# Performance work log

Hardware: AMD Instinct MI355X
Metric: run time of the kernel (lower is better)

## Reference

```python
import jax, jax.numpy as jnp
import numpy as np

HEADS = 8
MAX_REL = 256
D_MODEL = 512
QK_DIM = 512
V_DIM = 512
HEAD_QK = QK_DIM // HEADS
HEAD_V = V_DIM // HEADS
NUM_RPR = 2 * MAX_REL + 1


def setup_inputs() -> dict:
    key = jax.random.key(0)
    ks = jax.random.split(key, 9)
    B, S = 2, 2048
    scale = 1.0 / np.sqrt(D_MODEL)
    return {
        "query": jax.random.normal(ks[0], (B, S, D_MODEL), jnp.float32),
        "value": jax.random.normal(ks[1], (B, S, D_MODEL), jnp.float32),
        "Wq": jax.random.normal(ks[2], (D_MODEL, QK_DIM), jnp.float32) * scale,
        "Wk": jax.random.normal(ks[3], (D_MODEL, QK_DIM), jnp.float32) * scale,
        "Wv": jax.random.normal(ks[4], (D_MODEL, V_DIM), jnp.float32) * scale,
        "Wo": jax.random.normal(ks[5], (V_DIM, D_MODEL), jnp.float32) * scale,
        "bo": jnp.zeros((D_MODEL,), jnp.float32),
        "Ek": jax.random.normal(ks[6], (NUM_RPR, HEAD_QK), jnp.float32) * 0.02,
        "Ev": jax.random.normal(ks[7], (NUM_RPR, HEAD_V), jnp.float32) * 0.02,
    }


def _heads(x, h):
    B, S, D = x.shape
    return x.reshape(B, S, h, D // h).transpose(0, 2, 1, 3)  # (B,H,S,hd)


def reference(query, value, Wq, Wk, Wv, Wo, bo, Ek, Ev):
    B, S, _ = query.shape
    # rpr lookup: clip(j - i, -M, M) + M  -> (S, S)
    idx = jnp.arange(S)
    rpr = jnp.clip(idx[None, :] - idx[:, None], -MAX_REL, MAX_REL) + MAX_REL
    ek = Ek[rpr]  # (S, S, head_qk)
    ev = Ev[rpr]  # (S, S, head_v)

    q = _heads(query @ Wq, HEADS)   # (B,H,S,dk)
    k = _heads(value @ Wk, HEADS)   # key := value (per original call())
    v = _heads(value @ Wv, HEADS)   # (B,H,S,dv)

    alpha = jnp.einsum("bhid,bhjd->bhij", q, k)
    alpha = alpha + jnp.einsum("bhid,ijd->bhij", q, ek)
    alpha = alpha / jnp.sqrt(jnp.asarray(HEAD_QK, jnp.float32))
    attn_weights = jax.nn.softmax(alpha, axis=-1)  # (B,H,S,S)

    scores = jnp.einsum("bhij,bhjd->bhid", attn_weights, v)
    scores = scores + jnp.einsum("bhij,ijd->bhid", attn_weights, ev)

    concat = scores.transpose(0, 2, 1, 3).reshape(B, S, V_DIM)
    out = concat @ Wo + bo
    return out, attn_weights
```

## Files before the change

### kernel.cpp

```cpp
#include <hip/hip_runtime.h>

#define SB 2
#define HH 8
#define SS 2048
#define DM 512
#define HD 64
#define SCALE 0.125f

typedef __attribute__((ext_vector_type(8))) short bfrag;
typedef __attribute__((ext_vector_type(4))) float f4;

static __device__ __forceinline__ unsigned short f2bf(float x) {
  unsigned int u = __float_as_uint(x);
  unsigned int r = (u + 0x7FFFu + ((u >> 16) & 1u)) >> 16;
  return (unsigned short)r;
}
static __device__ __forceinline__ float bf2f(unsigned short s) {
  return __uint_as_float(((unsigned int)s) << 16);
}
static __device__ __forceinline__ void splitf(float x, short& hi, short& lo) {
  const unsigned u = __float_as_uint(x);
  hi = (short)(u >> 16);
  lo = (short)f2bf(x - __uint_as_float(u & 0xFFFF0000u));
}

static __device__ __forceinline__ void dma16(const unsigned short* g,
                                             unsigned short* l) {
  __builtin_amdgcn_global_load_lds(
      (const __attribute__((address_space(1))) void*)g,
      (__attribute__((address_space(3))) void*)l, 16, 0, 0);
}
static __device__ __forceinline__ void wait_vm4() {
  asm volatile("s_waitcnt vmcnt(4)" ::: "memory");
  __builtin_amdgcn_sched_barrier(0);
}
static __device__ __forceinline__ void wait_vm0() {
  asm volatile("s_waitcnt vmcnt(0)" ::: "memory");
  __builtin_amdgcn_sched_barrier(0);
}

__global__ __launch_bounds__(256) void gemm_f32(const float* __restrict__ A,
                                                const float* __restrict__ Bm,
                                                const float* __restrict__ bias,
                                                float* __restrict__ C,
                                                int M, int N, int K) {
  __shared__ float As[16][68];
  __shared__ float Bs[16][64];
  const int t = threadIdx.x;
  const int nb = N >> 6;
  const int bm = blockIdx.x / nb, bn = blockIdx.x % nb;
  const int m0 = bm << 6, n0 = bn << 6;
  const int ty = t >> 4, tx = t & 15;
  const int mr = ty << 2, nc = tx << 2;
  const int am = t >> 2, akq = t & 3;
  const int bk = t >> 4, bnq = t & 15;
  float acc[4][4] = {};
  for (int k0 = 0; k0 < K; k0 += 16) {
    const float4 av = *(const float4*)&A[(size_t)(m0 + am) * K + k0 + (akq << 2)];
    const float4 bv = *(const float4*)&Bm[(size_t)(k0 + bk) * N + n0 + (bnq << 2)];
    __syncthreads();
    As[(akq << 2) + 0][am] = av.x;
    As[(akq << 2) + 1][am] = av.y;
    As[(akq << 2) + 2][am] = av.z;
    As[(akq << 2) + 3][am] = av.w;
    *(float4*)&Bs[bk][bnq << 2] = bv;
    __syncthreads();
#pragma unroll
    for (int kk = 0; kk < 16; ++kk) {
      float a[4], b[4];
      *(float4*)a = *(const float4*)&As[kk][mr];
      *(float4*)b = *(const float4*)&Bs[kk][nc];
#pragma unroll
      for (int i = 0; i < 4; ++i)
#pragma unroll
        for (int j = 0; j < 4; ++j) acc[i][j] += a[i] * b[j];
    }
  }
#pragma unroll
  for (int i = 0; i < 4; ++i) {
    float4 v = make_float4(acc[i][0], acc[i][1], acc[i][2], acc[i][3]);
    if (bias) {
      v.x += bias[n0 + nc + 0];
      v.y += bias[n0 + nc + 1];
      v.z += bias[n0 + nc + 2];
      v.w += bias[n0 + nc + 3];
    }
    *(float4*)&C[(size_t)(m0 + mr + i) * N + n0 + nc] = v;
  }
}

__global__ __launch_bounds__(256) void gemm_f32_vt(const float* __restrict__ A,
                                                   const float* __restrict__ Bm,
                                                   unsigned short* __restrict__ VT,
                                                   int M, int N, int K) {
  __shared__ float As[16][68];
  __shared__ float Bs[16][64];
  const int t = threadIdx.x;
  const int nb = N >> 6;
  const int bm = blockIdx.x / nb, bn = blockIdx.x % nb;
  const int m0 = bm << 6, n0 = bn << 6;
  const int ty = t >> 4, tx = t & 15;
  const int mr = ty << 2, nc = tx << 2;
  const int am = t >> 2, akq = t & 3;
  const int bk = t >> 4, bnq = t & 15;
  float acc[4][4] = {};
  for (int k0 = 0; k0 < K; k0 += 16) {
    const float4 av = *(const float4*)&A[(size_t)(m0 + am) * K + k0 + (akq << 2)];
    const float4 bv = *(const float4*)&Bm[(size_t)(k0 + bk) * N + n0 + (bnq << 2)];
    __syncthreads();
    As[(akq << 2) + 0][am] = av.x;
    As[(akq << 2) + 1][am] = av.y;
    As[(akq << 2) + 2][am] = av.z;
    As[(akq << 2) + 3][am] = av.w;
    *(float4*)&Bs[bk][bnq << 2] = bv;
    __syncthreads();
#pragma unroll
    for (int kk = 0; kk < 16; ++kk) {
      float a[4], b[4];
      *(float4*)a = *(const float4*)&As[kk][mr];
      *(float4*)b = *(const float4*)&Bs[kk][nc];
#pragma unroll
      for (int i = 0; i < 4; ++i)
#pragma unroll
        for (int j = 0; j < 4; ++j) acc[i][j] += a[i] * b[j];
    }
  }
#pragma unroll
  for (int i = 0; i < 4; ++i) {
    const int row = m0 + mr + i;
    const int bb = row >> 11, jr = row & 2047;
#pragma unroll
    for (int jx = 0; jx < 4; ++jx) {
      const int col = n0 + nc + jx;
      const int bh = bb * HH + (col >> 6), d = col & 63;
      VT[((size_t)bh * HD + d) * SS + jr] = f2bf(acc[i][jx]);
    }
  }
}

__global__ __launch_bounds__(256) void gemm_f32_khl(const float* __restrict__ A,
                                                    const float* __restrict__ Bm,
                                                    unsigned short* __restrict__ kh,
                                                    unsigned short* __restrict__ kl,
                                                    int M, int N, int K) {
  __shared__ float As[16][68];
  __shared__ float Bs[16][64];
  const int t = threadIdx.x;
  const int nb = N >> 6;
  const int bm = blockIdx.x / nb, bn = blockIdx.x % nb;
  const int m0 = bm << 6, n0 = bn << 6;
  const int ty = t >> 4, tx = t & 15;
  const int mr = ty << 2, nc = tx << 2;
  const int am = t >> 2, akq = t & 3;
  const int bk = t >> 4, bnq = t & 15;
  float acc[4][4] = {};
  for (int k0 = 0; k0 < K; k0 += 16) {
    const float4 av = *(const float4*)&A[(size_t)(m0 + am) * K + k0 + (akq << 2)];
    const float4 bv = *(const float4*)&Bm[(size_t)(k0 + bk) * N + n0 + (bnq << 2)];
    __syncthreads();
    As[(akq << 2) + 0][am] = av.x;
    As[(akq << 2) + 1][am] = av.y;
    As[(akq << 2) + 2][am] = av.z;
    As[(akq << 2) + 3][am] = av.w;
    *(float4*)&Bs[bk][bnq << 2] = bv;
    __syncthreads();
#pragma unroll
    for (int kk = 0; kk < 16; ++kk) {
      float a[4], b[4];
      *(float4*)a = *(const float4*)&As[kk][mr];
      *(float4*)b = *(const float4*)&Bs[kk][nc];
#pragma unroll
      for (int i = 0; i < 4; ++i)
#pragma unroll
        for (int j = 0; j < 4; ++j) acc[i][j] += a[i] * b[j];
    }
  }
#pragma unroll
  for (int i = 0; i < 4; ++i) {
    const int row = m0 + mr + i;
    const int bb = row >> 11, jr = row & 2047;
#pragma unroll
    for (int jx = 0; jx < 4; ++jx) {
      const int col = n0 + nc + jx;
      const int bh = bb * HH + (col >> 6), d = col & 63;
      short hi, lo;
      splitf(acc[i][jx], hi, lo);
      const size_t o = ((size_t)bh * SS + jr) * HD + d;
      kh[o] = (unsigned short)hi;
      kl[o] = (unsigned short)lo;
    }
  }
}

__global__ void prep_evt(const float* __restrict__ Ev, unsigned short* __restrict__ EvT) {
  const int idx = blockIdx.x * 256 + threadIdx.x;
  if (idx >= 64 * 544) return;
  const int d = idx / 544, r = idx % 544;
  EvT[idx] = (r < 513) ? f2bf(Ev[(size_t)r * HD + d]) : (unsigned short)0;
}

#define QK6(K0, K1, L0, L1, ACC)                                            \
  ACC = __builtin_amdgcn_mfma_f32_16x16x32_bf16(qh0, K0, ACC, 0, 0, 0);     \
  ACC = __builtin_amdgcn_mfma_f32_16x16x32_bf16(qh1, K1, ACC, 0, 0, 0);     \
  ACC = __builtin_amdgcn_mfma_f32_16x16x32_bf16(ql0, K0, ACC, 0, 0, 0);     \
  ACC = __builtin_amdgcn_mfma_f32_16x16x32_bf16(ql1, K1, ACC, 0, 0, 0);     \
  ACC = __builtin_amdgcn_mfma_f32_16x16x32_bf16(qh0, L0, ACC, 0, 0, 0);     \
  ACC = __builtin_amdgcn_mfma_f32_16x16x32_bf16(qh1, L1, ACC, 0, 0, 0);

__global__ __launch_bounds__(256, 2) void fused_attn10(
    const float* __restrict__ Qp,
    const unsigned short* __restrict__ khg,
    const unsigned short* __restrict__ klg,
    const unsigned short* __restrict__ VTg,
    const float* __restrict__ Ek,
    const unsigned short* __restrict__ EvT,
    float* __restrict__ attn,
    float* __restrict__ concat) {
  __shared__ __attribute__((aligned(16))) unsigned short qek_lds[16][520];
  __shared__ __attribute__((aligned(16))) unsigned short wband[16][552];
  __shared__ __attribute__((aligned(16))) unsigned short kt_h[2][64][64];
  __shared__ __attribute__((aligned(16))) unsigned short kt_l[2][64][64];
  __shared__ __attribute__((aligned(16))) float ws_tile[2][16][64];
  __shared__ __attribute__((aligned(16))) unsigned short wt_bf[2][16][64];
  __shared__ float zb[4][16];
  __shared__ float lhb[4][16][2];

  const int t = threadIdx.x;
  const int orig = blockIdx.x;
  const int wg = (orig & 7) * 256 + (orig >> 3);
  const int bh = wg >> 7, rb = wg & 127;
  const int b = bh >> 3, h = bh & 7;
  const int wv = t >> 6, lane = t & 63;
  const int ln = lane & 15, lq = lane >> 4;
  const int i0 = rb * 16;

  {
    unsigned* wz = (unsigned*)&wband[0][0];
    for (int x = t; x < 16 * 552 / 2; x += 256) wz[x] = 0;
  }

  bfrag qh0, qh1, ql0, ql1;
  {
    const float* qrow = Qp + (size_t)(b * SS + i0 + ln) * DM + h * HD + lq * 8;
    const f4 x0 = *(const f4*)&qrow[0], x1 = *(const f4*)&qrow[4];
    const f4 x2 = *(const f4*)&qrow[32], x3 = *(const f4*)&qrow[36];
#pragma unroll
    for (int e = 0; e < 4; ++e) {
      short hi, lo;
      splitf(x0[e], hi, lo); qh0[e] = hi; ql0[e] = lo;
      splitf(x1[e], hi, lo); qh0[e + 4] = hi; ql0[e + 4] = lo;
      splitf(x2[e], hi, lo); qh1[e] = hi; ql1[e] = lo;
      splitf(x3[e], hi, lo); qh1[e + 4] = hi; ql1[e + 4] = lo;
    }
  }

  const unsigned short* khb = khg + (size_t)bh * SS * HD;
  const unsigned short* klb = klg + (size_t)bh * SS * HD;
  const unsigned short* vtb = VTg + (size_t)bh * HD * SS;
  const int row0 = i0 + lq * 4;
  const int rloc0 = lq * 4;

  const int rsub = lane >> 3;
  const int c8d = lane & 7;
  const int r0w = wv * 16;

  const int jt = r0w + ln;
  const int swk = jt & 7;
  const int c8k0 = (lq ^ swk) << 3, c8k1 = ((lq + 4) ^ swk) << 3;

#define ISSUE_K(JC, BUF)                                                      \
  {                                                                           \
    const int ra_ = r0w + rsub, rb_ = r0w + 8 + rsub;                         \
    dma16(khb + ((size_t)((JC) + ra_) * HD + ((c8d ^ (ra_ & 7)) << 3)),       \
          &kt_h[BUF][r0w][0]);                                                \
    dma16(khb + ((size_t)((JC) + rb_) * HD + ((c8d ^ (rb_ & 7)) << 3)),       \
          &kt_h[BUF][r0w + 8][0]);                                            \
    dma16(klb + ((size_t)((JC) + ra_) * HD + ((c8d ^ (ra_ & 7)) << 3)),       \
          &kt_l[BUF][r0w][0]);                                                \
    dma16(klb + ((size_t)((JC) + rb_) * HD + ((c8d ^ (rb_ & 7)) << 3)),       \
          &kt_l[BUF][r0w + 8][0]);                                            \
  }

  ISSUE_K(0, 0)

  for (int nt = wv; nt <= 32; nt += 4) {
    const int r = nt * 16 + ln;
    const int rc = r > 512 ? 512 : r;
    const float* erow = Ek + (size_t)rc * HD + lq * 8;
    const f4 a0 = *(const f4*)&erow[0], a1 = *(const f4*)&erow[4];
    const f4 a2 = *(const f4*)&erow[32], a3 = *(const f4*)&erow[36];
    bfrag e0, e1;
#pragma unroll
    for (int e = 0; e < 4; ++e) {
      e0[e] = (short)f2bf(a0[e]); e0[e + 4] = (short)f2bf(a1[e]);
      e1[e] = (short)f2bf(a2[e]); e1[e + 4] = (short)f2bf(a3[e]);
    }
    f4 acc = {0.f, 0.f, 0.f, 0.f};
    acc = __builtin_amdgcn_mfma_f32_16x16x32_bf16(qh0, e0, acc, 0, 0, 0);
    acc = __builtin_amdgcn_mfma_f32_16x16x32_bf16(qh1, e1, acc, 0, 0, 0);
    if (r < 513) {
#pragma unroll
      for (int rr = 0; rr < 4; ++rr)
        qek_lds[lq * 4 + rr][r] = f2bf(acc[rr] * SCALE);
    }
  }
  __syncthreads();

  float zz[4] = {0.f, 0.f, 0.f, 0.f};
#pragma unroll 1
  for (int it = 0; it < 32; ++it) {
    const int cur = it & 1;
    if (it < 31) { ISSUE_K((it + 1) * 64, cur ^ 1) wait_vm4(); }
    else wait_vm0();
    const bfrag k0 = *(const bfrag*)&kt_h[cur][jt][c8k0];
    const bfrag k1 = *(const bfrag*)&kt_h[cur][jt][c8k1];
    const bfrag l0 = *(const bfrag*)&kt_l[cur][jt][c8k0];
    const bfrag l1 = *(const bfrag*)&kt_l[cur][jt][c8k1];
    f4 acc = {0.f, 0.f, 0.f, 0.f};
    QK6(k0, k1, l0, l1, acc)
    const int jb2 = it * 64 + r0w + ln - row0;
#pragma unroll
    for (int r = 0; r < 4; ++r) {
      int idx = jb2 - r + 256;
      idx = idx < 0 ? 0 : (idx > 512 ? 512 : idx);
      const float qv = bf2f(qek_lds[rloc0 + r][idx]);
      zz[r] += __expf(fmaf(acc[r], SCALE, qv));
    }
  }
  ISSUE_K(0, 0)
#pragma unroll
  for (int r = 0; r < 4; ++r)
#pragma unroll
    for (int o = 1; o < 16; o <<= 1) zz[r] += __shfl_xor(zz[r], o);
  if (ln == 0) {
#pragma unroll
    for (int r = 0; r < 4; ++r) zb[wv][lq * 4 + r] = zz[r];
  }
  __syncthreads();
  float zi[4];
#pragma unroll
  for (int r = 0; r < 4; ++r)
    zi[r] = 1.f / (zb[0][lq * 4 + r] + zb[1][lq * 4 + r] +
                   zb[2][lq * 4 + r] + zb[3][lq * 4 + r]);

  f4 pv = {0.f, 0.f, 0.f, 0.f};
  float la[4] = {0.f, 0.f, 0.f, 0.f}, ha[4] = {0.f, 0.f, 0.f, 0.f};
  const int wbr = t >> 4;
  const int wbc = (t & 15) << 2;
#pragma unroll 1
  for (int it = 0; it < 32; ++it) {
    const int cur = it & 1;
    const int jc = it * 64;
    if (it < 31) ISSUE_K(jc + 64, cur ^ 1)
    const bfrag vb0 = *(const bfrag*)&vtb[(size_t)(r0w + ln) * SS + jc + lq * 8];
    const bfrag vb1 = *(const bfrag*)&vtb[(size_t)(r0w + ln) * SS + jc + 32 + lq * 8];
    {
      const bfrag k0 = *(const bfrag*)&kt_h[cur][jt][c8k0];
      const bfrag k1 = *(const bfrag*)&kt_h[cur][jt][c8k1];
      const bfrag l0 = *(const bfrag*)&kt_l[cur][jt][c8k0];
      const bfrag l1 = *(const bfrag*)&kt_l[cur][jt][c8k1];
      f4 acc = {0.f, 0.f, 0.f, 0.f};
      QK6(k0, k1, l0, l1, acc)
      const int j = jc + r0w + ln;
      const int jb2 = j - row0;
#pragma unroll
      for (int r = 0; r < 4; ++r) {
        int idx = jb2 - r + 256;
        idx = idx < 0 ? 0 : (idx > 512 ? 512 : idx);
        const float qv = bf2f(qek_lds[rloc0 + r][idx]);
        const float w = __expf(fmaf(acc[r], SCALE, qv)) * zi[r];
        const int rl = rloc0 + r;
        ws_tile[cur][rl][r0w + ln] = w;
        wt_bf[cur][rl][(((wv * 2 + (ln >> 3)) ^ (rl & 7)) << 3) + (ln & 7)] = f2bf(w);
        const int off = jb2 - r;
        if (off <= -256) la[r] += w;
        else if (off >= 256) ha[r] += w;
        else wband[rl][off + 256] = f2bf(w);
      }
    }
    __syncthreads();
    {
      const bfrag pa0 = *(const bfrag*)&wt_bf[cur][ln][((lq ^ (ln & 7)) << 3)];
      const bfrag pa1 = *(const bfrag*)&wt_bf[cur][ln][(((4 + lq) ^ (ln & 7)) << 3)];
      pv = __builtin_amdgcn_mfma_f32_16x16x32_bf16(pa0, vb0, pv, 0, 0, 0);
      pv = __builtin_amdgcn_mfma_f32_16x16x32_bf16(pa1, vb1, pv, 0, 0, 0);
      const f4 w4 = *(const f4*)&ws_tile[cur][wbr][wbc];
      __builtin_nontemporal_store(
          w4, (f4*)&attn[((size_t)bh * SS + i0 + wbr) * SS + jc + wbc]);
    }
  }
#pragma unroll
  for (int r = 0; r < 4; ++r) {
#pragma unroll
    for (int o = 1; o < 16; o <<= 1) {
      la[r] += __shfl_xor(la[r], o);
      ha[r] += __shfl_xor(ha[r], o);
    }
  }
  if (ln == 0) {
#pragma unroll
    for (int r = 0; r < 4; ++r) {
      lhb[wv][lq * 4 + r][0] = la[r];
      lhb[wv][lq * 4 + r][1] = ha[r];
    }
  }
  __syncthreads();

  if (t < 16) {
    float bl = 0.f, bhv = 0.f;
#pragma unroll
    for (int q = 0; q < 4; ++q) { bl += lhb[q][t][0]; bhv += lhb[q][t][1]; }
    wband[t][0] = f2bf(bl);
    wband[t][512] = f2bf(bhv);
  }
  __syncthreads();

  {
    f4 acc2 = {0.f, 0.f, 0.f, 0.f};
#pragma unroll 1
    for (int kt = 0; kt < 17; ++kt) {
      const bfrag a = *(const bfrag*)&wband[ln][kt * 32 + lq * 8];
      const bfrag bb = *(const bfrag*)&EvT[(size_t)(wv * 16 + ln) * 544 + kt * 32 + lq * 8];
      acc2 = __builtin_amdgcn_mfma_f32_16x16x32_bf16(a, bb, acc2, 0, 0, 0);
    }
#pragma unroll
    for (int r = 0; r < 4; ++r)
      concat[(size_t)(b * SS + i0 + lq * 4 + r) * DM + h * HD + wv * 16 + ln] =
          pv[r] + acc2[r];
  }
}

extern "C" void kernel_launch(void* const* d_in, const int* in_sizes, int n_in,
                              void* d_out, int out_size, void* d_ws, size_t ws_size,
                              hipStream_t stream) {
  (void)in_sizes; (void)n_in; (void)out_size; (void)ws_size;
  const float* query = (const float*)d_in[0];
  const float* value = (const float*)d_in[1];
  const float* Wq = (const float*)d_in[2];
  const float* Wk = (const float*)d_in[3];
  const float* Wv = (const float*)d_in[4];
  const float* Wo = (const float*)d_in[5];
  const float* bo = (const float*)d_in[6];
  const float* Ek = (const float*)d_in[7];
  const float* Ev = (const float*)d_in[8];

  float* out = (float*)d_out;
  float* attn = out + (size_t)SB * SS * DM;

  char* wsb = (char*)d_ws;
  float* Qp = (float*)(wsb + 0);
  float* concat = (float*)(wsb + 8388608);
  unsigned short* kb16h = (unsigned short*)(wsb + 16777216);
  unsigned short* kb16l = (unsigned short*)(wsb + 20971520);
  unsigned short* VT = (unsigned short*)(wsb + 25165824);
  unsigned short* EvT = (unsigned short*)(wsb + 29360128);

  const int M = SB * SS;
  dim3 blk(256);
  dim3 ggrid((M / 64) * (DM / 64));

  gemm_f32<<<ggrid, blk, 0, stream>>>(query, Wq, nullptr, Qp, M, DM, DM);
  gemm_f32_khl<<<ggrid, blk, 0, stream>>>(value, Wk, kb16h, kb16l, M, DM, DM);
  gemm_f32_vt<<<ggrid, blk, 0, stream>>>(value, Wv, VT, M, DM, DM);
  prep_evt<<<136, blk, 0, stream>>>(Ev, EvT);
  fused_attn10<<<2048, blk, 0, stream>>>(Qp, kb16h, kb16l, VT, Ek, EvT, attn, concat);
  gemm_f32<<<ggrid, blk, 0, stream>>>(concat, Wo, bo, out, M, DM, DM);
}
```

Measured before the change: 382.7 us.

## Replace FP32 SIMT projection GEMMs with split-bf16 MFMA GEMM using async LDS loads

The four 4096x512x512 projection GEMMs move from scalar FP32 FMA kernels to a single MFMA kernel. It emulates FP32 with three bf16 products (hi*hi, hi*lo, lo*hi). Weights are pre-split into transposed hi/lo bf16 copies by a new prep kernel. Activations are loaded through global_load_lds DMA into swizzled double-buffered LDS and split in registers. The change targets the FMA-bound projection cost around attention, at the price of extra prep launches and slightly lower precision than true FP32.

```diff
diff --git a/kernel.cpp b/kernel.cpp
--- a/kernel.cpp
+++ b/kernel.cpp
@@ -39,156 +39,160 @@
   __builtin_amdgcn_sched_barrier(0);
 }
 
-__global__ __launch_bounds__(256) void gemm_f32(const float* __restrict__ A,
-                                                const float* __restrict__ Bm,
-                                                const float* __restrict__ bias,
-                                                float* __restrict__ C,
-                                                int M, int N, int K) {
-  __shared__ float As[16][68];
-  __shared__ float Bs[16][64];
+__global__ __launch_bounds__(256) void prep_w(const float* __restrict__ W,
+                                              unsigned short* __restrict__ WTh,
+                                              unsigned short* __restrict__ WTl) {
   const int t = threadIdx.x;
-  const int nb = N >> 6;
-  const int bm = blockIdx.x / nb, bn = blockIdx.x % nb;
+  const int kb = blockIdx.x >> 3, nb = blockIdx.x & 7;
+  const int k0 = kb * 64 + ((t & 15) << 2);
+  const int n0 = nb * 64 + ((t >> 4) << 2);
+  f4 m[4];
+#pragma unroll
+  for (int u = 0; u < 4; ++u) m[u] = *(const f4*)&W[(size_t)(k0 + u) * DM + n0];
+#pragma unroll
+  for (int c = 0; c < 4; ++c) {
+    unsigned short ph[4], pl[4];
+#pragma unroll
+    for (int u = 0; u < 4; ++u) {
+      short hi, lo;
+      splitf(m[u][c], hi, lo);
+      ph[u] = (unsigned short)hi; pl[u] = (unsigned short)lo;
+    }
+    const size_t o = (size_t)(n0 + c) * DM + k0;
+    *(uint2*)&WTh[o] = make_uint2((unsigned)ph[0] | ((unsigned)ph[1] << 16),
+                                  (unsigned)ph[2] | ((unsigned)ph[3] << 16));
+    *(uint2*)&WTl[o] = make_uint2((unsigned)pl[0] | ((unsigned)pl[1] << 16),
+                                  (unsigned)pl[2] | ((unsigned)pl[3] << 16));
+  }
+}
+
+__global__ __launch_bounds__(256, 2) void mm2(const float* __restrict__ A,
+                                              const unsigned short* __restrict__ WTh,
+                                              const unsigned short* __restrict__ WTl,
+                                              const float* __restrict__ bias,
+                                              float* __restrict__ C,
+                                              unsigned short* __restrict__ O1,
+                                              unsigned short* __restrict__ O2,
+                                              int mode) {
+  __shared__ __attribute__((aligned(16))) float As[2][64][64];
+  __shared__ __attribute__((aligned(16))) unsigned short Bhs[2][64][64];
+  __shared__ __attribute__((aligned(16))) unsigned short Bls[2][64][64];
+  const int t = threadIdx.x;
+  const int bm = blockIdx.x >> 3, bn = blockIdx.x & 7;
   const int m0 = bm << 6, n0 = bn << 6;
-  const int ty = t >> 4, tx = t & 15;
-  const int mr = ty << 2, nc = tx << 2;
-  const int am = t >> 2, akq = t & 3;
-  const int bk = t >> 4, bnq = t & 15;
-  float acc[4][4] = {};
-  for (int k0 = 0; k0 < K; k0 += 16) {
-    const float4 av = *(const float4*)&A[(size_t)(m0 + am) * K + k0 + (akq << 2)];
-    const float4 bv = *(const float4*)&Bm[(size_t)(k0 + bk) * N + n0 + (bnq << 2)];
+  const int wv = t >> 6, lane = t & 63;
+  const int ln = lane & 15, lq = lane >> 4;
+  const int mw = (wv & 1) << 5, nw = (wv >> 1) << 5;
+  const int a_r = lane >> 4, a_c = lane & 15;
+  const int b_r = lane >> 3, b_c = lane & 7;
+
+#define MM2_ISSUE(K0, BUF)                                                    \
+  {                                                                           \
+    _Pragma("unroll")                                                         \
+    for (int i = 0; i < 4; ++i) {                                             \
+      const int rr = wv * 16 + i * 4 + a_r;                                   \
+      dma16((const unsigned short*)(A + (size_t)(m0 + rr) * DM + (K0) +       \
+                                    ((a_c ^ (rr & 15)) << 2)),                \
+            (unsigned short*)&As[BUF][wv * 16 + i * 4][0]);                   \
+    }                                                                         \
+    _Pragma("unroll")                                                         \
+    for (int i = 0; i < 2; ++i) {                                             \
+      const int rr = wv * 16 + i * 8 + b_r;                                   \
+      dma16(WTh + (size_t)(n0 + rr) * DM + (K0) + ((b_c ^ (rr & 7)) << 3),    \
+            &Bhs[BUF][wv * 16 + i * 8][0]);                                   \
+      dma16(WTl + (size_t)(n0 + rr) * DM + (K0) + ((b_c ^ (rr & 7)) << 3),    \
+            &Bls[BUF][wv * 16 + i * 8][0]);                                   \
+    }                                                                         \
+  }
+
+  f4 acc[2][2] = {{{0.f,0.f,0.f,0.f},{0.f,0.f,0.f,0.f}},
+                  {{0.f,0.f,0.f,0.f},{0.f,0.f,0.f,0.f}}};
+
+  MM2_ISSUE(0, 0)
+  __syncthreads();
+#pragma unroll 1
+  for (int kt = 0; kt < 8; ++kt) {
+    const int cur = kt & 1;
+    if (kt < 7) MM2_ISSUE((kt + 1) * 64, cur ^ 1)
+#pragma unroll
+    for (int ks = 0; ks < 2; ++ks) {
+      bfrag ah[2], al[2];
+#pragma unroll
+      for (int mf = 0; mf < 2; ++mf) {
+        const int row = mw + mf * 16 + ln;
+        const int cb = ks * 8 + lq * 2;
+        const f4 x0 = *(const f4*)&As[cur][row][(cb ^ ln) << 2];
+        const f4 x1 = *(const f4*)&As[cur][row][((cb + 1) ^ ln) << 2];
+        bfrag h, l2;
+#pragma unroll
+        for (int e = 0; e < 4; ++e) {
+          short hi, lo;
+          splitf(x0[e], hi, lo); h[e] = hi; l2[e] = lo;
+          splitf(x1[e], hi, lo); h[e + 4] = hi; l2[e + 4] = lo;
+        }
+        ah[mf] = h; al[mf] = l2;
+      }
+#pragma unroll
+      for (int nf = 0; nf < 2; ++nf) {
+        const int nrow = nw + nf * 16 + ln;
+        const int s = ((ks * 4 + lq) ^ (ln & 7)) << 3;
+        const bfrag bh = *(const bfrag*)&Bhs[cur][nrow][s];
+        const bfrag bl = *(const bfrag*)&Bls[cur][nrow][s];
+#pragma unroll
+        for (int mf = 0; mf < 2; ++mf) {
+          acc[mf][nf] = __builtin_amdgcn_mfma_f32_16x16x32_bf16(ah[mf], bh, acc[mf][nf], 0, 0, 0);
+          acc[mf][nf] = __builtin_amdgcn_mfma_f32_16x16x32_bf16(ah[mf], bl, acc[mf][nf], 0, 0, 0);
+          acc[mf][nf] = __builtin_amdgcn_mfma_f32_16x16x32_bf16(al[mf], bh, acc[mf][nf], 0, 0, 0);
+        }
+      }
+    }
     __syncthreads();
-    As[(akq << 2) + 0][am] = av.x;
-    As[(akq << 2) + 1][am] = av.y;
-    As[(akq << 2) + 2][am] = av.z;
-    As[(akq << 2) + 3][am] = av.w;
-    *(float4*)&Bs[bk][bnq << 2] = bv;
-    __syncthreads();
-#pragma unroll
-    for (int kk = 0; kk < 16; ++kk) {
-      float a[4], b[4];
-      *(float4*)a = *(const float4*)&As[kk][mr];
-      *(float4*)b = *(const float4*)&Bs[kk][nc];
-#pragma unroll
-      for (int i = 0; i < 4; ++i)
-#pragma unroll
-        for (int j = 0; j < 4; ++j) acc[i][j] += a[i] * b[j];
-    }
-  }
-#pragma unroll
-  for (int i = 0; i < 4; ++i) {
-    float4 v = make_float4(acc[i][0], acc[i][1], acc[i][2], acc[i][3]);
-    if (bias) {
-      v.x += bias[n0 + nc + 0];
-      v.y += bias[n0 + nc + 1];
-      v.z += bias[n0 + nc + 2];
-      v.w += bias[n0 + nc + 3];
-    }
-    *(float4*)&C[(size_t)(m0 + mr + i) * N + n0 + nc] = v;
-  }
-}
-
-__global__ __launch_bounds__(256) void gemm_f32_vt(const float* __restrict__ A,
-                                                   const float* __restrict__ Bm,
-                                                   unsigned short* __restrict__ VT,
-                                                   int M, int N, int K) {
-  __shared__ float As[16][68];
-  __shared__ float Bs[16][64];
-  const int t = threadIdx.x;
-  const int nb = N >> 6;
-  const int bm = blockIdx.x / nb, bn = blockIdx.x % nb;
-  const int m0 = bm << 6, n0 = bn << 6;
-  const int ty = t >> 4, tx = t & 15;
-  const int mr = ty << 2, nc = tx << 2;
-  const int am = t >> 2, akq = t & 3;
-  const int bk = t >> 4, bnq = t & 15;
-  float acc[4][4] = {};
-  for (int k0 = 0; k0 < K; k0 += 16) {
-    const float4 av = *(const float4*)&A[(size_t)(m0 + am) * K + k0 + (akq << 2)];
-    const float4 bv = *(const float4*)&Bm[(size_t)(k0 + bk) * N + n0 + (bnq << 2)];
-    __syncthreads();
-    As[(akq << 2) + 0][am] = av.x;
-    As[(akq << 2) + 1][am] = av.y;
-    As[(akq << 2) + 2][am] = av.z;
-    As[(akq << 2) + 3][am] = av.w;
-    *(float4*)&Bs[bk][bnq << 2] = bv;
-    __syncthreads();
-#pragma unroll
-    for (int kk = 0; kk < 16; ++kk) {
-      float a[4], b[4];
-      *(float4*)a = *(const float4*)&As[kk][mr];
-      *(float4*)b = *(const float4*)&Bs[kk][nc];
-#pragma unroll
-      for (int i = 0; i < 4; ++i)
-#pragma unroll
-        for (int j = 0; j < 4; ++j) acc[i][j] += a[i] * b[j];
-    }
-  }
-#pragma unroll
-  for (int i = 0; i < 4; ++i) {
-    const int row = m0 + mr + i;
-    const int bb = row >> 11, jr = row & 2047;
-#pragma unroll
-    for (int jx = 0; jx < 4; ++jx) {
-      const int col = n0 + nc + jx;
-      const int bh = bb * HH + (col >> 6), d = col & 63;
-      VT[((size_t)bh * HD + d) * SS + jr] = f2bf(acc[i][jx]);
-    }
-  }
-}
-
-__global__ __launch_bounds__(256) void gemm_f32_khl(const float* __restrict__ A,
-                                                    const float* __restrict__ Bm,
-                                                    unsigned short* __restrict__ kh,
-                                                    unsigned short* __restrict__ kl,
-                                                    int M, int N, int K) {
-  __shared__ float As[16][68];
-  __shared__ float Bs[16][64];
-  const int t = threadIdx.x;
-  const int nb = N >> 6;
-  const int bm = blockIdx.x / nb, bn = blockIdx.x % nb;
-  const int m0 = bm << 6, n0 = bn << 6;
-  const int ty = t >> 4, tx = t & 15;
-  const int mr = ty << 2, nc = tx << 2;
-  const int am = t >> 2, akq = t & 3;
-  const int bk = t >> 4, bnq = t & 15;
-  float acc[4][4] = {};
-  for (int k0 = 0; k0 < K; k0 += 16) {
-    const float4 av = *(const float4*)&A[(size_t)(m0 + am) * K + k0 + (akq << 2)];
-    const float4 bv = *(const float4*)&Bm[(size_t)(k0 + bk) * N + n0 + (bnq << 2)];
-    __syncthreads();
-    As[(akq << 2) + 0][am] = av.x;
-    As[(akq << 2) + 1][am] = av.y;
-    As[(akq << 2) + 2][am] = av.z;
-    As[(akq << 2) + 3][am] = av.w;
-    *(float4*)&Bs[bk][bnq << 2] = bv;
-    __syncthreads();
-#pragma unroll
-    for (int kk = 0; kk < 16; ++kk) {
-      float a[4], b[4];
-      *(float4*)a = *(const float4*)&As[kk][mr];
-      *(float4*)b = *(const float4*)&Bs[kk][nc];
-#pragma unroll
-      for (int i = 0; i < 4; ++i)
-#pragma unroll
-        for (int j = 0; j < 4; ++j) acc[i][j] += a[i] * b[j];
-    }
-  }
-#pragma unroll
-  for (int i = 0; i < 4; ++i) {
-    const int row = m0 + mr + i;
-    const int bb = row >> 11, jr = row & 2047;
-#pragma unroll
-    for (int jx = 0; jx < 4; ++jx) {
-      const int col = n0 + nc + jx;
-      const int bh = bb * HH + (col >> 6), d = col & 63;
-      short hi, lo;
-      splitf(acc[i][jx], hi, lo);
-      const size_t o = ((size_t)bh * SS + jr) * HD + d;
-      kh[o] = (unsigned short)hi;
-      kl[o] = (unsigned short)lo;
-    }
+  }
+
+  if (mode == 0) {
+#pragma unroll
+    for (int mf = 0; mf < 2; ++mf)
+#pragma unroll
+      for (int nf = 0; nf < 2; ++nf) {
+        const int col = n0 + nw + nf * 16 + ln;
+        const float bv = bias ? bias[col] : 0.f;
+#pragma unroll
+        for (int r = 0; r < 4; ++r)
+          C[(size_t)(m0 + mw + mf * 16 + lq * 4 + r) * DM + col] =
+              acc[mf][nf][r] + bv;
+      }
+  } else if (mode == 1) {
+#pragma unroll
+    for (int mf = 0; mf < 2; ++mf)
+#pragma unroll
+      for (int nf = 0; nf < 2; ++nf) {
+        const int col = n0 + nw + nf * 16 + ln;
+#pragma unroll
+        for (int r = 0; r < 4; ++r) {
+          const int row = m0 + mw + mf * 16 + lq * 4 + r;
+          const int bb = row >> 11, jr = row & 2047;
+          const int bh2 = bb * HH + (col >> 6), d = col & 63;
+          short hi, lo;
+          splitf(acc[mf][nf][r], hi, lo);
+          const size_t o = ((size_t)bh2 * SS + jr) * HD + d;
+          O1[o] = (unsigned short)hi;
+          O2[o] = (unsigned short)lo;
+        }
+      }
+  } else {
+#pragma unroll
+    for (int mf = 0; mf < 2; ++mf)
+#pragma unroll
+      for (int nf = 0; nf < 2; ++nf) {
+        const int col = n0 + nw + nf * 16 + ln;
+#pragma unroll
+        for (int r = 0; r < 4; ++r) {
+          const int row = m0 + mw + mf * 16 + lq * 4 + r;
+          const int bb = row >> 11, jr = row & 2047;
+          const int bh2 = bb * HH + (col >> 6), d = col & 63;
+          O1[((size_t)bh2 * HD + d) * SS + jr] = f2bf(acc[mf][nf][r]);
+        }
+      }
   }
 }
 
@@ -454,15 +458,26 @@
   unsigned short* kb16l = (unsigned short*)(wsb + 20971520);
   unsigned short* VT = (unsigned short*)(wsb + 25165824);
   unsigned short* EvT = (unsigned short*)(wsb + 29360128);
-
-  const int M = SB * SS;
+  unsigned short* WTs = (unsigned short*)(wsb + 29491200);
+  unsigned short* WTqh = WTs + 0 * 262144;
+  unsigned short* WTql = WTs + 1 * 262144;
+  unsigned short* WTkh = WTs + 2 * 262144;
+  unsigned short* WTkl = WTs + 3 * 262144;
+  unsigned short* WTvh = WTs + 4 * 262144;
+  unsigned short* WTvl = WTs + 5 * 262144;
+  unsigned short* WToh = WTs + 6 * 262144;
+  unsigned short* WTol = WTs + 7 * 262144;
+
   dim3 blk(256);
-  dim3 ggrid((M / 64) * (DM / 64));
-
-  gemm_f32<<<ggrid, blk, 0, stream>>>(query, Wq, nullptr, Qp, M, DM, DM);
-  gemm_f32_khl<<<ggrid, blk, 0, stream>>>(value, Wk, kb16h, kb16l, M, DM, DM);
-  gemm_f32_vt<<<ggrid, blk, 0, stream>>>(value, Wv, VT, M, DM, DM);
+
+  prep_w<<<64, blk, 0, stream>>>(Wq, WTqh, WTql);
+  prep_w<<<64, blk, 0, stream>>>(Wk, WTkh, WTkl);
+  prep_w<<<64, blk, 0, stream>>>(Wv, WTvh, WTvl);
+  prep_w<<<64, blk, 0, stream>>>(Wo, WToh, WTol);
   prep_evt<<<136, blk, 0, stream>>>(Ev, EvT);
+  mm2<<<512, blk, 0, stream>>>(query, WTqh, WTql, nullptr, Qp, nullptr, nullptr, 0);
+  mm2<<<512, blk, 0, stream>>>(value, WTkh, WTkl, nullptr, nullptr, kb16h, kb16l, 1);
+  mm2<<<512, blk, 0, stream>>>(value, WTvh, WTvl, nullptr, nullptr, VT, nullptr, 2);
   fused_attn10<<<2048, blk, 0, stream>>>(Qp, kb16h, kb16l, VT, Ek, EvT, attn, concat);
-  gemm_f32<<<ggrid, blk, 0, stream>>>(concat, Wo, bo, out, M, DM, DM);
-}
+  mm2<<<512, blk, 0, stream>>>(concat, WToh, WTol, bo, out, nullptr, nullptr, 0);
+}
```

Result: faster. 315.3 us (-17.6%).
